# Performance work log

Measured on AMD Instinct MI355X. Metric: run time of the kernel, lower is better.

Reference implementation:

```python
import jax, jax.numpy as jnp
import numpy as np

B, L, D, V, K, H, HD, FFN = 64, 512, 256, 32000, 6, 4, 64, 512

def _ln(x, g, b):
    mu = x.mean(-1, keepdims=True)
    v = ((x - mu) ** 2).mean(-1, keepdims=True)
    return (x - mu) / jnp.sqrt(v + 1e-5) * g + b

def _pool(x, mask):
    # attention pooling: last real token attends over full sequence
    lengths = mask.sum(1)
    last = jnp.maximum(lengths - 1, 0)
    q = x[jnp.arange(x.shape[0]), last]                      # [B,D]
    scores = jnp.einsum('bd,bld->bl', q, x)
    scores = jnp.where(mask, scores, -60000.0)
    a = jax.nn.softmax(scores, axis=-1)
    return jnp.einsum('bl,bld->bd', a, x)

def _expert(x, mask, ln1g, ln1b, Wqkv, bqkv, Wo, bo, ln2g, ln2b, W1, b1, W2, b2):
    # pre-LN transformer block, eval mode (dropout = identity)
    Bx, Lx, _ = x.shape
    h = _ln(x, ln1g, ln1b)
    qkv = h @ Wqkv.T + bqkv                                   # [B,L,3D]
    q, k, v = jnp.split(qkv, 3, axis=-1)
    q = q.reshape(Bx, Lx, H, HD).transpose(0, 2, 1, 3)
    k = k.reshape(Bx, Lx, H, HD).transpose(0, 2, 1, 3)
    v = v.reshape(Bx, Lx, H, HD).transpose(0, 2, 1, 3)
    s = jnp.einsum('bhqd,bhkd->bhqk', q, k) / jnp.sqrt(jnp.float32(HD))
    s = jnp.where(mask[:, None, None, :], s, -1e9)            # key_padding_mask
    a = jax.nn.softmax(s, axis=-1)
    o = jnp.einsum('bhqk,bhkd->bhqd', a, v).transpose(0, 2, 1, 3).reshape(Bx, Lx, D)
    x = x + o @ Wo.T + bo
    h2 = _ln(x, ln2g, ln2b)
    ff = jax.nn.gelu(h2 @ W1.T + b1, approximate=False) @ W2.T + b2
    return x + ff

def _gru(z, m, Wih, Whh, bih, bhh):
    # torch.nn.GRUCell semantics
    gi = z @ Wih.T + bih
    gh = m @ Whh.T + bhh
    ir, iz, inn = jnp.split(gi, 3, axis=-1)
    hr, hz, hn = jnp.split(gh, 3, axis=-1)
    r = jax.nn.sigmoid(ir + hr)
    u = jax.nn.sigmoid(iz + hz)
    n = jnp.tanh(inn + r * hn)
    return (1.0 - u) * n + u * m

def setup_inputs():
    key = jax.random.key(0)
    ks = jax.random.split(key, 24)
    def nrm(k, shape, s=0.02):
        return jax.random.normal(k, shape, jnp.float32) * s
    lengths = jax.random.randint(ks[0], (B,), 1, L + 1)
    mask = jnp.arange(L)[None, :] < lengths[:, None]          # prefix mask, >=1 real token
    tokens = jnp.where(mask, jax.random.randint(ks[1], (B, L), 1, V), 0)
    return dict(
        tokens=tokens, mask=mask,
        tok_emb=nrm(ks[2], (V, D)).at[0].set(0.0),            # padding_idx=0
        pos_emb=nrm(ks[3], (L, D)),
        emb_ln_g=jnp.ones((D,)), emb_ln_b=jnp.zeros((D,)),
        ln1_g=jnp.ones((K, D)), ln1_b=jnp.zeros((K, D)),
        Wqkv=nrm(ks[4], (K, 3 * D, D)), bqkv=jnp.zeros((K, 3 * D)),
        Wo=nrm(ks[5], (K, D, D)), bo=jnp.zeros((K, D)),
        ln2_g=jnp.ones((K, D)), ln2_b=jnp.zeros((K, D)),
        W1=nrm(ks[6], (K, FFN, D)), b1=jnp.zeros((K, FFN)),
        W2=nrm(ks[7], (K, D, FFN)), b2=jnp.zeros((K, D)),
        gru_Wih=nrm(ks[8], (3 * D, D)), gru_Whh=nrm(ks[9], (3 * D, D)),
        gru_bih=jnp.zeros((3 * D,)), gru_bhh=jnp.zeros((3 * D,)),
        cls_W=nrm(ks[10], (V, D)), cls_b=jnp.zeros((V,)),
    )

def reference(tokens, mask, tok_emb, pos_emb, emb_ln_g, emb_ln_b, ln1_g, ln1_b, Wqkv, bqkv, Wo, bo, ln2_g, ln2_b, W1, b1, W2, b2, gru_Wih, gru_Whh, gru_bih, gru_bhh, cls_W, cls_b):
    x = _ln(tok_emb[tokens] + pos_emb[None, :tokens.shape[1]], emb_ln_g, emb_ln_b)
    m = jnp.zeros((tokens.shape[0], D), x.dtype)
    # sequential routing / phase-1: n_iter = K, chosen = t % K for all samples, no halting
    for t in range(K):
        e = t % K
        x = _expert(x, mask, ln1_g[e], ln1_b[e], Wqkv[e], bqkv[e], Wo[e], bo[e],
                    ln2_g[e], ln2_b[e], W1[e], b1[e], W2[e], b2[e])
        z = _pool(x, mask)
        m = _gru(z, m, gru_Wih, gru_Whh, gru_bih, gru_bhh)    # GRU memory update
    return _pool(x, mask) @ cls_W.T + cls_b                   # [B, V] logits
```

## Files before the change

kernel.cpp:

```cpp
#include <hip/hip_runtime.h>
#include <hip/hip_bf16.h>

#define BB 64
#define LL 512
#define DD 256
#define VV 32000
#define KK 6
#define HH 4
#define FF 512
#define MM (BB * LL)

typedef __hip_bfloat16 bf16;
typedef unsigned short ushort_t;
typedef __attribute__((ext_vector_type(8))) __bf16 bf16x8;
typedef __attribute__((ext_vector_type(4))) float f32x4;
#define MFMA __builtin_amdgcn_mfma_f32_16x16x32_bf16

__device__ __forceinline__ ushort_t f2bfbits(float x) {
  return __builtin_bit_cast(unsigned short, (__bf16)x);
}
__device__ __forceinline__ unsigned pkbf(float lo, float hi) {
  return (unsigned)f2bfbits(lo) | ((unsigned)f2bfbits(hi) << 16);
}
union U8 { unsigned u[4]; bf16x8 v; };

__device__ __forceinline__ void gl_lds16(const ushort_t* g, ushort_t* l) {
  __builtin_amdgcn_global_load_lds(
      (const __attribute__((address_space(1))) unsigned int*)g,
      (__attribute__((address_space(3))) unsigned int*)l, 16, 0, 0);
}

__device__ __forceinline__ float blk_sum(float v, float* red) {
  #pragma unroll
  for (int o = 32; o > 0; o >>= 1) v += __shfl_down(v, o, 64);
  __syncthreads();
  if ((threadIdx.x & 63) == 0) red[threadIdx.x >> 6] = v;
  __syncthreads();
  return red[0] + red[1] + red[2] + red[3];
}

__global__ __launch_bounds__(256) void k_lens(const int* __restrict__ tokens, int* __restrict__ lens) {
  __shared__ float red[4];
  int b = blockIdx.x, t = threadIdx.x;
  float c = (tokens[b * LL + t] != 0 ? 1.f : 0.f) + (tokens[b * LL + 256 + t] != 0 ? 1.f : 0.f);
  float s = blk_sum(c, red);
  if (t == 0) lens[b] = (int)(s + 0.5f);
}

__global__ __launch_bounds__(256) void k_embed4(const int* __restrict__ tokens,
                                                const float* __restrict__ tok_emb,
                                                const float* __restrict__ pos_emb,
                                                const float* __restrict__ g,
                                                const float* __restrict__ be,
                                                float* __restrict__ X) {
  int wid = threadIdx.x >> 6, lane = threadIdx.x & 63;
  int row = blockIdx.x * 4 + wid;
  int l = row & (LL - 1);
  int tok = tokens[row];
  float4 a = *reinterpret_cast<const float4*>(tok_emb + (size_t)tok * DD + lane * 4);
  float4 p = *reinterpret_cast<const float4*>(pos_emb + (size_t)l * DD + lane * 4);
  float4 v = {a.x + p.x, a.y + p.y, a.z + p.z, a.w + p.w};
  float s = v.x + v.y + v.z + v.w;
  float q = v.x * v.x + v.y * v.y + v.z * v.z + v.w * v.w;
  #pragma unroll
  for (int o = 32; o > 0; o >>= 1) { s += __shfl_xor(s, o, 64); q += __shfl_xor(q, o, 64); }
  float mu = s * (1.f / DD);
  float rstd = rsqrtf(q * (1.f / DD) - mu * mu + 1e-5f);
  float4 gv = *reinterpret_cast<const float4*>(g + lane * 4);
  float4 bv = *reinterpret_cast<const float4*>(be + lane * 4);
  float4 o4 = {(v.x - mu) * rstd * gv.x + bv.x, (v.y - mu) * rstd * gv.y + bv.y,
               (v.z - mu) * rstd * gv.z + bv.z, (v.w - mu) * rstd * gv.w + bv.w};
  *reinterpret_cast<float4*>(X + (size_t)row * DD + lane * 4) = o4;
}

__global__ __launch_bounds__(256) void k_ln4(const float* __restrict__ X,
                                             const float* __restrict__ g,
                                             const float* __restrict__ be,
                                             const int* __restrict__ lens,
                                             bf16* __restrict__ H) {
  int wid = threadIdx.x >> 6, lane = threadIdx.x & 63;
  int row = blockIdx.x * 4 + wid;
  int b = row >> 9, l = row & (LL - 1);
  if (l >= lens[b]) return;
  float4 v = *reinterpret_cast<const float4*>(X + (size_t)row * DD + lane * 4);
  float s = v.x + v.y + v.z + v.w;
  float q = v.x * v.x + v.y * v.y + v.z * v.z + v.w * v.w;
  #pragma unroll
  for (int o = 32; o > 0; o >>= 1) { s += __shfl_xor(s, o, 64); q += __shfl_xor(q, o, 64); }
  float mu = s * (1.f / DD);
  float rstd = rsqrtf(q * (1.f / DD) - mu * mu + 1e-5f);
  float4 gv = *reinterpret_cast<const float4*>(g + lane * 4);
  float4 bv = *reinterpret_cast<const float4*>(be + lane * 4);
  ushort4 o4;
  o4.x = f2bfbits((v.x - mu) * rstd * gv.x + bv.x);
  o4.y = f2bfbits((v.y - mu) * rstd * gv.y + bv.y);
  o4.z = f2bfbits((v.z - mu) * rstd * gv.z + bv.z);
  o4.w = f2bfbits((v.w - mu) * rstd * gv.w + bv.w);
  *reinterpret_cast<ushort4*>((ushort_t*)H + (size_t)row * DD + lane * 4) = o4;
}

__global__ __launch_bounds__(256) void k_cvtw(const float* __restrict__ w0, const float* __restrict__ w1,
                                              const float* __restrict__ w2, const float* __restrict__ w3,
                                              ushort_t* __restrict__ d) {
  int i = (blockIdx.x * 256 + threadIdx.x) * 4;
  const float* s; int off;
  if (i < 196608)      { s = w0; off = i; }
  else if (i < 262144) { s = w1; off = i - 196608; }
  else if (i < 393216) { s = w2; off = i - 262144; }
  else                 { s = w3; off = i - 393216; }
  float4 v = *reinterpret_cast<const float4*>(s + off);
  ushort4 o;
  o.x = f2bfbits(v.x); o.y = f2bfbits(v.y); o.z = f2bfbits(v.z); o.w = f2bfbits(v.w);
  *reinterpret_cast<ushort4*>(d + i) = o;
}

template <int MT, int NT, int KD, bool GELU, bool RES, bool OUTBF16>
__global__ __launch_bounds__(256) void k_mgemm(const ushort_t* __restrict__ A,
                                               const ushort_t* __restrict__ Wb,
                                               const float* __restrict__ bias,
                                               const float* __restrict__ res,
                                               void* __restrict__ outp,
                                               const int* __restrict__ lens,
                                               int Ndim) {
  constexpr int JF = (MT == 128) ? (NT / 32) : (NT / 64);
  constexpr int AR = MT / 64, BR = NT / 64;
  constexpr int L = AR + BR;
  constexpr int NK = KD / 32;
  int n0 = blockIdx.x * NT, m0 = blockIdx.y * MT;
  if ((m0 & (LL - 1)) >= lens[m0 >> 9]) return;
  __shared__ __align__(16) ushort_t As[3][MT * 32];
  __shared__ __align__(16) ushort_t Bs[3][NT * 32];
  int t = threadIdx.x, lane = t & 63, w = t >> 6;
  int wr = (MT == 128) ? (w >> 1) * 64 : 0;
  int wc = (MT == 128) ? (w & 1) * (NT / 2) : w * (NT / 4);
  int fr = lane & 15, fg = lane >> 4;

  int ca = lane & 3;
  const ushort_t* gA[AR];
  #pragma unroll
  for (int ra = 0; ra < AR; ra++) {
    int row = ra * 64 + (t >> 2);
    gA[ra] = A + (size_t)(m0 + row) * KD + ((ca ^ ((row >> 1) & 3)) << 3);
  }
  const ushort_t* gB[BR];
  #pragma unroll
  for (int rb = 0; rb < BR; rb++) {
    int row = rb * 64 + (t >> 2);
    gB[rb] = Wb + (size_t)(n0 + row) * KD + ((ca ^ ((row >> 1) & 3)) << 3);
  }

  f32x4 acc[4][JF];
  #pragma unroll
  for (int i = 0; i < 4; i++)
    #pragma unroll
    for (int j = 0; j < JF; j++) acc[i][j] = (f32x4){0.f, 0.f, 0.f, 0.f};

  #define STAGE(bi, koff) { \
    _Pragma("unroll") for (int ra = 0; ra < AR; ra++) gl_lds16(gA[ra] + (koff), &As[bi][ra * 2048 + w * 512]); \
    _Pragma("unroll") for (int rb = 0; rb < BR; rb++) gl_lds16(gB[rb] + (koff), &Bs[bi][rb * 2048 + w * 512]); }

  STAGE(0, 0);
  #pragma unroll
  for (int kt = 0; kt < NK; kt++) {
    int cur = kt % 3;
    if (kt + 1 < NK) {
      STAGE((kt + 1) % 3, (kt + 1) * 32);
      asm volatile("s_waitcnt vmcnt(%0)" :: "n"(L) : "memory");
    } else {
      asm volatile("s_waitcnt vmcnt(0)" ::: "memory");
    }
    __builtin_amdgcn_s_barrier();
    __builtin_amdgcn_sched_barrier(0);
    bf16x8 af[4], bfr[JF];
    #pragma unroll
    for (int i = 0; i < 4; i++) {
      int row = wr + i * 16 + fr;
      af[i] = *reinterpret_cast<const bf16x8*>(&As[cur][row * 32 + ((fg ^ ((row >> 1) & 3)) << 3)]);
    }
    #pragma unroll
    for (int j = 0; j < JF; j++) {
      int row = wc + j * 16 + fr;
      bfr[j] = *reinterpret_cast<const bf16x8*>(&Bs[cur][row * 32 + ((fg ^ ((row >> 1) & 3)) << 3)]);
    }
    #pragma unroll
    for (int i = 0; i < 4; i++)
      #pragma unroll
      for (int j = 0; j < JF; j++)
        acc[i][j] = MFMA(af[i], bfr[j], acc[i][j], 0, 0, 0);
  }
  #undef STAGE

  #pragma unroll
  for (int i = 0; i < 4; i++) {
    int mbase = m0 + wr + i * 16 + fg * 4;
    #pragma unroll
    for (int j = 0; j < JF; j++) {
      int n = n0 + wc + j * 16 + fr;
      float bs = bias[n];
      #pragma unroll
      for (int r = 0; r < 4; r++) {
        int m = mbase + r;
        float v = acc[i][j][r] + bs;
        if (RES) v += res[(size_t)m * Ndim + n];
        if (GELU) v = 0.5f * v * (1.f + erff(v * 0.70710678118f));
        if (OUTBF16) ((ushort_t*)outp)[(size_t)m * Ndim + n] = f2bfbits(v);
        else         ((float*)outp)[(size_t)m * Ndim + n] = v;
      }
    }
  }
}

__global__ __launch_bounds__(512) void k_mattn6(const ushort_t* __restrict__ QKV,
                                                const int* __restrict__ lens,
                                                ushort_t* __restrict__ O) {
  int b = blockIdx.z, h = blockIdx.y;
  int len = lens[b];
  int q0 = blockIdx.x * 128;
  if (q0 >= len) return;
  int t = threadIdx.x, lane = t & 63, w = t >> 6;
  int fr = lane & 15, fg = lane >> 4;
  __shared__ __align__(16) ushort_t Kh[8192];
  __shared__ __align__(16) ushort_t Vh[8192];

  const ushort_t* base = QKV + (size_t)b * LL * 768;
  int qw = q0 + w * 16;
  bool qact = qw < len;
  int q = qw + fr;

  const ushort_t* qp = base + (size_t)q * 768 + h * 64 + fg * 8;
  bf16x8 qf0 = *reinterpret_cast<const bf16x8*>(qp);
  bf16x8 qf1 = *reinterpret_cast<const bf16x8*>(qp + 32);

  const float SC = 0.125f * 1.44269504f;
  f32x4 ot[4];
  #pragma unroll
  for (int df = 0; df < 4; df++) ot[df] = (f32x4){0.f, 0.f, 0.f, 0.f};
  float m_run = -1e30f, lsum = 0.f;

  for (int kb = 0; kb < len; kb += 128) {
    if (kb) __syncthreads();
    int lim = min(128, len - kb);
    #pragma unroll
    for (int rr = 0; rr < 2; rr++) {
      if (rr * 64 >= lim) break;
      int krow = rr * 64 + w * 8 + (lane >> 3);
      int gk = kb + krow; if (gk > len - 1) gk = len - 1;
      int ch = lane & 7;
      const ushort_t* src = base + (size_t)gk * 768 + 256 + h * 64 + ((ch ^ (krow & 7)) << 3);
      gl_lds16(src, &Kh[rr * 4096 + w * 512]);
    }
    #pragma unroll
    for (int it = 0; it < 2; it++) {
      if (it * 64 >= lim) break;
      int c = it * 512 + t;
      int k = c >> 3, dg = c & 7;
      int gk = kb + k; if (gk > len - 1) gk = len - 1;
      uint4 vv = *reinterpret_cast<const uint4*>(base + (size_t)gk * 768 + 512 + h * 64 + dg * 8);
      unsigned uu[4] = {vv.x, vv.y, vv.z, vv.w};
      #pragma unroll
      for (int j = 0; j < 4; j++) {
        int d0 = dg * 8 + j * 2, d1 = d0 + 1;
        int s0 = (d0 ^ (d0 >> 3)) & 7, s1 = (d1 ^ (d1 >> 3)) & 7;
        Vh[d0 * 128 + (((k >> 3) ^ s0) << 3) + (k & 7)] = (ushort_t)(uu[j] & 0xffff);
        Vh[d1 * 128 + (((k >> 3) ^ s1) << 3) + (k & 7)] = (ushort_t)(uu[j] >> 16);
      }
    }
    __syncthreads();

    if (qact) {
      for (int kt = 0; kt < lim; kt += 64) {
        f32x4 s[4];
        #pragma unroll
        for (int f = 0; f < 4; f++) {
          s[f] = (f32x4){0.f, 0.f, 0.f, 0.f};
          int krow = kt + f * 16 + fr;
          const ushort_t* kp0 = &Kh[krow * 64 + ((fg ^ (krow & 7)) << 3)];
          const ushort_t* kp1 = &Kh[krow * 64 + (((4 + fg) ^ (krow & 7)) << 3)];
          s[f] = MFMA(*reinterpret_cast<const bf16x8*>(kp0), qf0, s[f], 0, 0, 0);
          s[f] = MFMA(*reinterpret_cast<const bf16x8*>(kp1), qf1, s[f], 0, 0, 0);
        }
        int rem = lim - kt;
        #pragma unroll
        for (int f = 0; f < 4; f++)
          #pragma unroll
          for (int r = 0; r < 4; r++)
            s[f][r] = (f * 16 + fg * 4 + r < rem) ? s[f][r] * SC : -1e30f;
        float tm = -1e30f;
        #pragma unroll
        for (int f = 0; f < 4; f++)
          #pragma unroll
          for (int r = 0; r < 4; r++) tm = fmaxf(tm, s[f][r]);
        tm = fmaxf(tm, __shfl_xor(tm, 16, 64));
        tm = fmaxf(tm, __shfl_xor(tm, 32, 64));
        bool grow = tm > m_run;
        if (__any(grow)) {
          float m_new = grow ? tm : m_run;
          float corr = exp2f(m_run - m_new);
          lsum *= corr;
          #pragma unroll
          for (int df = 0; df < 4; df++)
            #pragma unroll
            for (int r = 0; r < 4; r++) ot[df][r] *= corr;
          m_run = m_new;
        }
        float ps = 0.f;
        #pragma unroll
        for (int f = 0; f < 4; f++)
          #pragma unroll
          for (int r = 0; r < 4; r++) {
            float p = exp2f(s[f][r] - m_run);
            s[f][r] = p; ps += p;
          }
        ps += __shfl_xor(ps, 16, 64);
        ps += __shfl_xor(ps, 32, 64);
        lsum += ps;
        #pragma unroll
        for (int st = 0; st < 2; st++) {
          int fA = st * 2, fB = fA + 1;
          unsigned a0 = pkbf(s[fA][0], s[fA][1]), a1 = pkbf(s[fA][2], s[fA][3]);
          unsigned b0 = pkbf(s[fB][0], s[fB][1]), b1 = pkbf(s[fB][2], s[fB][3]);
          int sA = ((fg & 1) * 2) * 16 + fr;
          int sB = sA + 16;
          unsigned wa0 = __shfl(a0, sA, 64), wb0 = __shfl(b0, sA, 64);
          unsigned wa1 = __shfl(a1, sA, 64), wb1 = __shfl(b1, sA, 64);
          unsigned wa2 = __shfl(a0, sB, 64), wb2 = __shfl(b0, sB, 64);
          unsigned wa3 = __shfl(a1, sB, 64), wb3 = __shfl(b1, sB, 64);
          bool lo = fg < 2;
          U8 pf;
          pf.u[0] = lo ? wa0 : wb0; pf.u[1] = lo ? wa1 : wb1;
          pf.u[2] = lo ? wa2 : wb2; pf.u[3] = lo ? wa3 : wb3;
          int cb = (kt >> 3) + st * 4 + fg;
          #pragma unroll
          for (int df = 0; df < 4; df++) {
            int d = df * 16 + fr;
            int sd = (d ^ (d >> 3)) & 7;
            const ushort_t* vp = &Vh[d * 128 + ((cb ^ sd) << 3)];
            ot[df] = MFMA(*reinterpret_cast<const bf16x8*>(vp), pf.v, ot[df], 0, 0, 0);
          }
        }
      }
    }
  }

  if (q < len) {
    float linv = 1.f / lsum;
    #pragma unroll
    for (int df = 0; df < 4; df++) {
      ushort4 ov;
      ov.x = f2bfbits(ot[df][0] * linv);
      ov.y = f2bfbits(ot[df][1] * linv);
      ov.z = f2bfbits(ot[df][2] * linv);
      ov.w = f2bfbits(ot[df][3] * linv);
      *reinterpret_cast<ushort4*>(O + (size_t)(b * LL + q) * DD + h * 64 + df * 16 + fg * 4) = ov;
    }
  }
}

__global__ __launch_bounds__(256) void k_pool(const float* __restrict__ X,
                                              const int* __restrict__ lens,
                                              bf16* __restrict__ pooled) {
  __shared__ float red[4];
  __shared__ float qs[DD];
  __shared__ float sc[LL];
  int b = blockIdx.x, t = threadIdx.x;
  int len = lens[b];
  const float* Xb = X + (size_t)b * LL * DD;
  qs[t] = Xb[(size_t)(len - 1) * DD + t];
  __syncthreads();
  for (int l = t; l < LL; l += 256) {
    float s = -1e30f;
    if (l < len) {
      const float4* xr = reinterpret_cast<const float4*>(Xb + (size_t)l * DD);
      const float4* qq = reinterpret_cast<const float4*>(qs);
      float a0 = 0, a1 = 0, a2 = 0, a3 = 0;
      for (int k4 = 0; k4 < 64; k4++) {
        float4 xv = xr[k4], qv = qq[k4];
        a0 += xv.x * qv.x; a1 += xv.y * qv.y; a2 += xv.z * qv.z; a3 += xv.w * qv.w;
      }
      s = (a0 + a1) + (a2 + a3);
    }
    sc[l] = s;
  }
  __syncthreads();
  float mx = fmaxf(sc[t], sc[t + 256]);
  #pragma unroll
  for (int off = 32; off > 0; off >>= 1) mx = fmaxf(mx, __shfl_down(mx, off, 64));
  __syncthreads();
  if ((t & 63) == 0) red[t >> 6] = mx;
  __syncthreads();
  mx = fmaxf(fmaxf(red[0], red[1]), fmaxf(red[2], red[3]));
  float e0 = (t < len) ? __expf(sc[t] - mx) : 0.f;
  float e1 = (t + 256 < len) ? __expf(sc[t + 256] - mx) : 0.f;
  float ssum = blk_sum(e0 + e1, red);
  float inv = 1.f / ssum;
  __syncthreads();
  sc[t] = e0 * inv; sc[t + 256] = e1 * inv;
  __syncthreads();
  float acc = 0.f;
  for (int l = 0; l < len; l++) acc += sc[l] * Xb[(size_t)l * DD + t];
  pooled[b * DD + t] = __float2bfloat16(acc);
}

__global__ __launch_bounds__(512) void k_cls(const ushort_t* __restrict__ POOL,
                                             const float* __restrict__ W,
                                             const float* __restrict__ bias,
                                             float* __restrict__ out) {
  int t = threadIdx.x, lane = t & 63, w = t >> 6;
  int fr = lane & 15, fg = lane >> 4;
  int n = blockIdx.x * 128 + w * 16 + fr;
  const float* wp = W + (size_t)n * DD + fg * 8;
  f32x4 acc[4];
  #pragma unroll
  for (int i = 0; i < 4; i++) acc[i] = (f32x4){0.f, 0.f, 0.f, 0.f};
  for (int k0 = 0; k0 < DD; k0 += 32) {
    float4 f0 = *reinterpret_cast<const float4*>(wp + k0);
    float4 f1 = *reinterpret_cast<const float4*>(wp + k0 + 4);
    U8 bfr;
    bfr.u[0] = pkbf(f0.x, f0.y); bfr.u[1] = pkbf(f0.z, f0.w);
    bfr.u[2] = pkbf(f1.x, f1.y); bfr.u[3] = pkbf(f1.z, f1.w);
    #pragma unroll
    for (int i = 0; i < 4; i++) {
      bf16x8 af = *reinterpret_cast<const bf16x8*>(POOL + (size_t)(i * 16 + fr) * DD + k0 + fg * 8);
      acc[i] = MFMA(af, bfr.v, acc[i], 0, 0, 0);
    }
  }
  float bs = bias[n];
  #pragma unroll
  for (int i = 0; i < 4; i++)
    #pragma unroll
    for (int r = 0; r < 4; r++)
      out[(size_t)(i * 16 + fg * 4 + r) * VV + n] = acc[i][r] + bs;
}

extern "C" void kernel_launch(void* const* d_in, const int* in_sizes, int n_in,
                              void* d_out, int out_size, void* d_ws, size_t ws_size,
                              hipStream_t stream) {
  const int*   tokens  = (const int*)d_in[0];
  const float* tok_emb = (const float*)d_in[2];
  const float* pos_emb = (const float*)d_in[3];
  const float* emb_g   = (const float*)d_in[4];
  const float* emb_b   = (const float*)d_in[5];
  const float* ln1_g   = (const float*)d_in[6];
  const float* ln1_b   = (const float*)d_in[7];
  const float* Wqkv    = (const float*)d_in[8];
  const float* bqkv    = (const float*)d_in[9];
  const float* Wo      = (const float*)d_in[10];
  const float* bo      = (const float*)d_in[11];
  const float* ln2_g   = (const float*)d_in[12];
  const float* ln2_b   = (const float*)d_in[13];
  const float* W1      = (const float*)d_in[14];
  const float* b1      = (const float*)d_in[15];
  const float* W2      = (const float*)d_in[16];
  const float* b2      = (const float*)d_in[17];
  const float* cls_W   = (const float*)d_in[22];
  const float* cls_b   = (const float*)d_in[23];

  char* ws = (char*)d_ws;
  float*    X    = (float*)ws;
  ushort_t* QKV  = (ushort_t*)(ws + 33554432);
  ushort_t* Hb   = (ushort_t*)(ws + 83886080);
  ushort_t* WB   = (ushort_t*)(ws + 100663296);
  ushort_t* POOL = (ushort_t*)(ws + 101711872);
  int*      LEN  = (int*)(ws + 101744640);

  const int OFF_QKV = 0, OFF_WO = 196608, OFF_W1 = 262144, OFF_W2 = 393216;

  k_lens<<<BB, 256, 0, stream>>>(tokens, LEN);
  k_embed4<<<MM / 4, 256, 0, stream>>>(tokens, tok_emb, pos_emb, emb_g, emb_b, X);

  for (int e = 0; e < KK; e++) {
    k_cvtw<<<512, 256, 0, stream>>>(Wqkv + (size_t)e * 196608, Wo + (size_t)e * 65536,
                                    W1 + (size_t)e * 131072, W2 + (size_t)e * 131072, WB);
    k_ln4<<<MM / 4, 256, 0, stream>>>(X, ln1_g + e * DD, ln1_b + e * DD, LEN, (bf16*)Hb);
    k_mgemm<128, 256, 256, false, false, true><<<dim3(3, 256), 256, 0, stream>>>(
        Hb, WB + OFF_QKV, bqkv + e * 3 * DD, nullptr, QKV, LEN, 3 * DD);
    k_mattn6<<<dim3(4, HH, BB), 512, 0, stream>>>(QKV, LEN, Hb);
    k_mgemm<64, 256, 256, false, true, false><<<dim3(1, 512), 256, 0, stream>>>(
        Hb, WB + OFF_WO, bo + e * DD, X, X, LEN, DD);
    k_ln4<<<MM / 4, 256, 0, stream>>>(X, ln2_g + e * DD, ln2_b + e * DD, LEN, (bf16*)Hb);
    k_mgemm<128, 256, 256, true, false, true><<<dim3(2, 256), 256, 0, stream>>>(
        Hb, WB + OFF_W1, b1 + e * FF, nullptr, QKV, LEN, FF);
    k_mgemm<64, 256, 512, false, true, false><<<dim3(1, 512), 256, 0, stream>>>(
        QKV, WB + OFF_W2, b2 + e * DD, X, X, LEN, DD);
  }

  k_pool<<<BB, 256, 0, stream>>>(X, LEN, (bf16*)POOL);
  k_cls<<<dim3(VV / 128), 512, 0, stream>>>(POOL, cls_W, cls_b, (float*)d_out);
}
```

Measured before the change: 879.5 us.

## Fuse LayerNorm into GEMM epilogues, sort attention batches by length, add MFMA priority

Removes the separate LayerNorm kernels by computing row mean and variance in the epilogue of the Wo and W2 residual GEMMs, which hold full 256-wide rows, and writing the normalized bf16 activations directly. The embedding kernel also emits the first LN1 output. Attention blocks are dispatched longest sequence first via a small sort kernel, use s_setprio around the MFMA sections, and skip the score mask on full key tiles. This saves two passes over the activations per layer and evens out attention load, at the cost of extra shared-memory reductions and barriers in the GEMM epilogue.

```diff
diff --git a/kernel.cpp b/kernel.cpp
--- a/kernel.cpp
+++ b/kernel.cpp
@@ -47,12 +47,29 @@
   if (t == 0) lens[b] = (int)(s + 0.5f);
 }
 
+__global__ __launch_bounds__(64) void k_order(const int* __restrict__ lens, int* __restrict__ order) {
+  int b = threadIdx.x;
+  __shared__ int L[64];
+  int len = lens[b];
+  L[b] = len;
+  __syncthreads();
+  int rank = 0;
+  for (int i = 0; i < 64; i++) {
+    int li = L[i];
+    if (li > len || (li == len && i < b)) rank++;
+  }
+  order[rank] = b;
+}
+
 __global__ __launch_bounds__(256) void k_embed4(const int* __restrict__ tokens,
                                                 const float* __restrict__ tok_emb,
                                                 const float* __restrict__ pos_emb,
                                                 const float* __restrict__ g,
                                                 const float* __restrict__ be,
-                                                float* __restrict__ X) {
+                                                const float* __restrict__ g1,
+                                                const float* __restrict__ b1,
+                                                float* __restrict__ X,
+                                                bf16* __restrict__ H) {
   int wid = threadIdx.x >> 6, lane = threadIdx.x & 63;
   int row = blockIdx.x * 4 + wid;
   int l = row & (LL - 1);
@@ -71,32 +88,20 @@
   float4 o4 = {(v.x - mu) * rstd * gv.x + bv.x, (v.y - mu) * rstd * gv.y + bv.y,
                (v.z - mu) * rstd * gv.z + bv.z, (v.w - mu) * rstd * gv.w + bv.w};
   *reinterpret_cast<float4*>(X + (size_t)row * DD + lane * 4) = o4;
-}
-
-__global__ __launch_bounds__(256) void k_ln4(const float* __restrict__ X,
-                                             const float* __restrict__ g,
-                                             const float* __restrict__ be,
-                                             const int* __restrict__ lens,
-                                             bf16* __restrict__ H) {
-  int wid = threadIdx.x >> 6, lane = threadIdx.x & 63;
-  int row = blockIdx.x * 4 + wid;
-  int b = row >> 9, l = row & (LL - 1);
-  if (l >= lens[b]) return;
-  float4 v = *reinterpret_cast<const float4*>(X + (size_t)row * DD + lane * 4);
-  float s = v.x + v.y + v.z + v.w;
-  float q = v.x * v.x + v.y * v.y + v.z * v.z + v.w * v.w;
-  #pragma unroll
-  for (int o = 32; o > 0; o >>= 1) { s += __shfl_xor(s, o, 64); q += __shfl_xor(q, o, 64); }
-  float mu = s * (1.f / DD);
-  float rstd = rsqrtf(q * (1.f / DD) - mu * mu + 1e-5f);
-  float4 gv = *reinterpret_cast<const float4*>(g + lane * 4);
-  float4 bv = *reinterpret_cast<const float4*>(be + lane * 4);
-  ushort4 o4;
-  o4.x = f2bfbits((v.x - mu) * rstd * gv.x + bv.x);
-  o4.y = f2bfbits((v.y - mu) * rstd * gv.y + bv.y);
-  o4.z = f2bfbits((v.z - mu) * rstd * gv.z + bv.z);
-  o4.w = f2bfbits((v.w - mu) * rstd * gv.w + bv.w);
-  *reinterpret_cast<ushort4*>((ushort_t*)H + (size_t)row * DD + lane * 4) = o4;
+  float s2 = o4.x + o4.y + o4.z + o4.w;
+  float q2 = o4.x * o4.x + o4.y * o4.y + o4.z * o4.z + o4.w * o4.w;
+  #pragma unroll
+  for (int o = 32; o > 0; o >>= 1) { s2 += __shfl_xor(s2, o, 64); q2 += __shfl_xor(q2, o, 64); }
+  float mu2 = s2 * (1.f / DD);
+  float rstd2 = rsqrtf(q2 * (1.f / DD) - mu2 * mu2 + 1e-5f);
+  float4 g1v = *reinterpret_cast<const float4*>(g1 + lane * 4);
+  float4 b1v = *reinterpret_cast<const float4*>(b1 + lane * 4);
+  ushort4 h4;
+  h4.x = f2bfbits((o4.x - mu2) * rstd2 * g1v.x + b1v.x);
+  h4.y = f2bfbits((o4.y - mu2) * rstd2 * g1v.y + b1v.y);
+  h4.z = f2bfbits((o4.z - mu2) * rstd2 * g1v.z + b1v.z);
+  h4.w = f2bfbits((o4.w - mu2) * rstd2 * g1v.w + b1v.w);
+  *reinterpret_cast<ushort4*>((ushort_t*)H + (size_t)row * DD + lane * 4) = h4;
 }
 
 __global__ __launch_bounds__(256) void k_cvtw(const float* __restrict__ w0, const float* __restrict__ w1,
@@ -114,12 +119,15 @@
   *reinterpret_cast<ushort4*>(d + i) = o;
 }
 
-template <int MT, int NT, int KD, bool GELU, bool RES, bool OUTBF16>
+template <int MT, int NT, int KD, bool GELU, bool RES, bool OUTBF16, bool FUSELN>
 __global__ __launch_bounds__(256) void k_mgemm(const ushort_t* __restrict__ A,
                                                const ushort_t* __restrict__ Wb,
                                                const float* __restrict__ bias,
                                                const float* __restrict__ res,
                                                void* __restrict__ outp,
+                                               ushort_t* __restrict__ Hout,
+                                               const float* __restrict__ lng,
+                                               const float* __restrict__ lnb,
                                                const int* __restrict__ lens,
                                                int Ndim) {
   constexpr int JF = (MT == 128) ? (NT / 32) : (NT / 64);
@@ -190,30 +198,94 @@
   }
   #undef STAGE
 
-  #pragma unroll
-  for (int i = 0; i < 4; i++) {
-    int mbase = m0 + wr + i * 16 + fg * 4;
-    #pragma unroll
-    for (int j = 0; j < JF; j++) {
-      int n = n0 + wc + j * 16 + fr;
-      float bs = bias[n];
+  if constexpr (!FUSELN) {
+    #pragma unroll
+    for (int i = 0; i < 4; i++) {
+      int mbase = m0 + wr + i * 16 + fg * 4;
+      #pragma unroll
+      for (int j = 0; j < JF; j++) {
+        int n = n0 + wc + j * 16 + fr;
+        float bs = bias[n];
+        #pragma unroll
+        for (int r = 0; r < 4; r++) {
+          int m = mbase + r;
+          float v = acc[i][j][r] + bs;
+          if (RES) v += res[(size_t)m * Ndim + n];
+          if (GELU) v = 0.5f * v * (1.f + erff(v * 0.70710678118f));
+          if (OUTBF16) ((ushort_t*)outp)[(size_t)m * Ndim + n] = f2bfbits(v);
+          else         ((float*)outp)[(size_t)m * Ndim + n] = v;
+        }
+      }
+    }
+  } else {
+    __shared__ float redS[4][64], redQ[4][64], lnmv[64], lnrv[64];
+    float rs[4][4], rq[4][4];
+    #pragma unroll
+    for (int i = 0; i < 4; i++)
+      #pragma unroll
+      for (int r = 0; r < 4; r++) { rs[i][r] = 0.f; rq[i][r] = 0.f; }
+    #pragma unroll
+    for (int i = 0; i < 4; i++) {
+      #pragma unroll
+      for (int j = 0; j < 4; j++) {
+        int n = wc + j * 16 + fr;
+        float bs = bias[n];
+        #pragma unroll
+        for (int r = 0; r < 4; r++) {
+          int m = m0 + i * 16 + fg * 4 + r;
+          float v = acc[i][j][r] + bs;
+          if (RES) v += res[(size_t)m * DD + n];
+          acc[i][j][r] = v;
+          ((float*)outp)[(size_t)m * DD + n] = v;
+          rs[i][r] += v; rq[i][r] += v * v;
+        }
+      }
+    }
+    #pragma unroll
+    for (int i = 0; i < 4; i++)
       #pragma unroll
       for (int r = 0; r < 4; r++) {
-        int m = mbase + r;
-        float v = acc[i][j][r] + bs;
-        if (RES) v += res[(size_t)m * Ndim + n];
-        if (GELU) v = 0.5f * v * (1.f + erff(v * 0.70710678118f));
-        if (OUTBF16) ((ushort_t*)outp)[(size_t)m * Ndim + n] = f2bfbits(v);
-        else         ((float*)outp)[(size_t)m * Ndim + n] = v;
-      }
-    }
-  }
-}
-
-__global__ __launch_bounds__(512) void k_mattn6(const ushort_t* __restrict__ QKV,
+        float s = rs[i][r], q = rq[i][r];
+        s += __shfl_xor(s, 1, 64); q += __shfl_xor(q, 1, 64);
+        s += __shfl_xor(s, 2, 64); q += __shfl_xor(q, 2, 64);
+        s += __shfl_xor(s, 4, 64); q += __shfl_xor(q, 4, 64);
+        s += __shfl_xor(s, 8, 64); q += __shfl_xor(q, 8, 64);
+        if (fr == 0) {
+          redS[w][i * 16 + fg * 4 + r] = s;
+          redQ[w][i * 16 + fg * 4 + r] = q;
+        }
+      }
+    __syncthreads();
+    if (t < 64) {
+      float s = redS[0][t] + redS[1][t] + redS[2][t] + redS[3][t];
+      float q = redQ[0][t] + redQ[1][t] + redQ[2][t] + redQ[3][t];
+      float mu = s * (1.f / DD);
+      lnmv[t] = mu;
+      lnrv[t] = rsqrtf(q * (1.f / DD) - mu * mu + 1e-5f);
+    }
+    __syncthreads();
+    #pragma unroll
+    for (int i = 0; i < 4; i++) {
+      #pragma unroll
+      for (int j = 0; j < 4; j++) {
+        int n = wc + j * 16 + fr;
+        float gv = lng[n], bv = lnb[n];
+        #pragma unroll
+        for (int r = 0; r < 4; r++) {
+          int rl = i * 16 + fg * 4 + r;
+          float h = (acc[i][j][r] - lnmv[rl]) * lnrv[rl] * gv + bv;
+          Hout[(size_t)(m0 + rl) * DD + n] = f2bfbits(h);
+        }
+      }
+    }
+  }
+}
+
+__global__ __launch_bounds__(512) void k_mattn7(const ushort_t* __restrict__ QKV,
                                                 const int* __restrict__ lens,
+                                                const int* __restrict__ order,
                                                 ushort_t* __restrict__ O) {
-  int b = blockIdx.z, h = blockIdx.y;
+  int b = order[blockIdx.z], h = blockIdx.y;
   int len = lens[b];
   int q0 = blockIdx.x * 128;
   if (q0 >= len) return;
@@ -270,6 +342,7 @@
     if (qact) {
       for (int kt = 0; kt < lim; kt += 64) {
         f32x4 s[4];
+        __builtin_amdgcn_s_setprio(1);
         #pragma unroll
         for (int f = 0; f < 4; f++) {
           s[f] = (f32x4){0.f, 0.f, 0.f, 0.f};
@@ -279,12 +352,20 @@
           s[f] = MFMA(*reinterpret_cast<const bf16x8*>(kp0), qf0, s[f], 0, 0, 0);
           s[f] = MFMA(*reinterpret_cast<const bf16x8*>(kp1), qf1, s[f], 0, 0, 0);
         }
-        int rem = lim - kt;
-        #pragma unroll
-        for (int f = 0; f < 4; f++)
+        __builtin_amdgcn_s_setprio(0);
+        if (lim - kt >= 64) {
           #pragma unroll
-          for (int r = 0; r < 4; r++)
-            s[f][r] = (f * 16 + fg * 4 + r < rem) ? s[f][r] * SC : -1e30f;
+          for (int f = 0; f < 4; f++)
+            #pragma unroll
+            for (int r = 0; r < 4; r++) s[f][r] *= SC;
+        } else {
+          int rem = lim - kt;
+          #pragma unroll
+          for (int f = 0; f < 4; f++)
+            #pragma unroll
+            for (int r = 0; r < 4; r++)
+              s[f][r] = (f * 16 + fg * 4 + r < rem) ? s[f][r] * SC : -1e30f;
+        }
         float tm = -1e30f;
         #pragma unroll
         for (int f = 0; f < 4; f++)
@@ -330,6 +411,7 @@
           pf.u[0] = lo ? wa0 : wb0; pf.u[1] = lo ? wa1 : wb1;
           pf.u[2] = lo ? wa2 : wb2; pf.u[3] = lo ? wa3 : wb3;
           int cb = (kt >> 3) + st * 4 + fg;
+          __builtin_amdgcn_s_setprio(1);
           #pragma unroll
           for (int df = 0; df < 4; df++) {
             int d = df * 16 + fr;
@@ -337,6 +419,7 @@
             const ushort_t* vp = &Vh[d * 128 + ((cb ^ sd) << 3)];
             ot[df] = MFMA(*reinterpret_cast<const bf16x8*>(vp), pf.v, ot[df], 0, 0, 0);
           }
+          __builtin_amdgcn_s_setprio(0);
         }
       }
     }
@@ -462,26 +545,33 @@
   ushort_t* WB   = (ushort_t*)(ws + 100663296);
   ushort_t* POOL = (ushort_t*)(ws + 101711872);
   int*      LEN  = (int*)(ws + 101744640);
+  int*      ORD  = (int*)(ws + 101744896);
 
   const int OFF_QKV = 0, OFF_WO = 196608, OFF_W1 = 262144, OFF_W2 = 393216;
 
   k_lens<<<BB, 256, 0, stream>>>(tokens, LEN);
-  k_embed4<<<MM / 4, 256, 0, stream>>>(tokens, tok_emb, pos_emb, emb_g, emb_b, X);
+  k_order<<<1, 64, 0, stream>>>(LEN, ORD);
+  k_embed4<<<MM / 4, 256, 0, stream>>>(tokens, tok_emb, pos_emb, emb_g, emb_b,
+                                       ln1_g, ln1_b, X, (bf16*)Hb);
 
   for (int e = 0; e < KK; e++) {
     k_cvtw<<<512, 256, 0, stream>>>(Wqkv + (size_t)e * 196608, Wo + (size_t)e * 65536,
                                     W1 + (size_t)e * 131072, W2 + (size_t)e * 131072, WB);
-    k_ln4<<<MM / 4, 256, 0, stream>>>(X, ln1_g + e * DD, ln1_b + e * DD, LEN, (bf16*)Hb);
-    k_mgemm<128, 256, 256, false, false, true><<<dim3(3, 256), 256, 0, stream>>>(
-        Hb, WB + OFF_QKV, bqkv + e * 3 * DD, nullptr, QKV, LEN, 3 * DD);
-    k_mattn6<<<dim3(4, HH, BB), 512, 0, stream>>>(QKV, LEN, Hb);
-    k_mgemm<64, 256, 256, false, true, false><<<dim3(1, 512), 256, 0, stream>>>(
-        Hb, WB + OFF_WO, bo + e * DD, X, X, LEN, DD);
-    k_ln4<<<MM / 4, 256, 0, stream>>>(X, ln2_g + e * DD, ln2_b + e * DD, LEN, (bf16*)Hb);
-    k_mgemm<128, 256, 256, true, false, true><<<dim3(2, 256), 256, 0, stream>>>(
-        Hb, WB + OFF_W1, b1 + e * FF, nullptr, QKV, LEN, FF);
-    k_mgemm<64, 256, 512, false, true, false><<<dim3(1, 512), 256, 0, stream>>>(
-        QKV, WB + OFF_W2, b2 + e * DD, X, X, LEN, DD);
+    k_mgemm<128, 256, 256, false, false, true, false><<<dim3(3, 256), 256, 0, stream>>>(
+        Hb, WB + OFF_QKV, bqkv + e * 3 * DD, nullptr, QKV, nullptr, nullptr, nullptr, LEN, 3 * DD);
+    k_mattn7<<<dim3(4, HH, BB), 512, 0, stream>>>(QKV, LEN, ORD, Hb);
+    k_mgemm<64, 256, 256, false, true, false, true><<<dim3(1, 512), 256, 0, stream>>>(
+        Hb, WB + OFF_WO, bo + e * DD, X, X, Hb, ln2_g + e * DD, ln2_b + e * DD, LEN, DD);
+    k_mgemm<128, 256, 256, true, false, true, false><<<dim3(2, 256), 256, 0, stream>>>(
+        Hb, WB + OFF_W1, b1 + e * FF, nullptr, QKV, nullptr, nullptr, nullptr, LEN, FF);
+    if (e < KK - 1) {
+      k_mgemm<64, 256, 512, false, true, false, true><<<dim3(1, 512), 256, 0, stream>>>(
+          QKV, WB + OFF_W2, b2 + e * DD, X, X, Hb,
+          ln1_g + (e + 1) * DD, ln1_b + (e + 1) * DD, LEN, DD);
+    } else {
+      k_mgemm<64, 256, 512, false, true, false, false><<<dim3(1, 512), 256, 0, stream>>>(
+          QKV, WB + OFF_W2, b2 + e * DD, X, X, nullptr, nullptr, nullptr, LEN, DD);
+    }
   }
 
   k_pool<<<BB, 256, 0, stream>>>(X, LEN, (bf16*)POOL);
```

Result: faster. 808.8 us (-8.0%).
